# Performance work log

Measured on AMD Instinct MI355X. Metric: run time of the kernel, lower is better.

The kernel has to match this reference:

```python
import jax, jax.numpy as jnp
import numpy as np

N_NODES = 100000
N_EDGES = 1600000
NODE_FEAT_DIM = 140
NUM_OPCODES = 128
EMBED_DIM = 64
HIDDEN = 128
N_LAYERS = 4
LN_EPS = 1e-5


def _layer_norm(x, g, b):
    mu = jnp.mean(x, axis=-1, keepdims=True)
    var = jnp.mean(jnp.square(x - mu), axis=-1, keepdims=True)
    return (x - mu) * jax.lax.rsqrt(var + LN_EPS) * g + b


def setup_inputs() -> dict:
    key = jax.random.key(0)
    ks = jax.random.split(key, 16)
    node_feat = jax.random.normal(ks[0], (N_NODES, NODE_FEAT_DIM), dtype=jnp.float32)
    node_opcode = jax.random.randint(ks[1], (N_NODES,), 0, NUM_OPCODES)
    topo_depth = jax.random.uniform(ks[2], (N_NODES, 1), dtype=jnp.float32)
    edge_index = jax.random.randint(ks[3], (2, N_EDGES), 0, N_NODES)
    in_dim = NODE_FEAT_DIM + EMBED_DIM + 1  # 205
    s_in = 1.0 / np.sqrt(in_dim)
    s_h = 1.0 / np.sqrt(HIDDEN)
    embed = jax.random.normal(ks[4], (NUM_OPCODES, EMBED_DIM), dtype=jnp.float32)
    embed = embed.at[0].set(0.0)  # padding_idx=0
    W_in = jax.random.uniform(ks[5], (in_dim, HIDDEN), minval=-s_in, maxval=s_in, dtype=jnp.float32)
    b_in = jax.random.uniform(ks[6], (HIDDEN,), minval=-s_in, maxval=s_in, dtype=jnp.float32)
    ln0_g = jnp.ones((HIDDEN,), jnp.float32)
    ln0_b = jnp.zeros((HIDDEN,), jnp.float32)
    # SAGEConv per layer: lin_l (neighbors, with bias), lin_r (self, no bias)
    Wl = jax.random.uniform(ks[7], (N_LAYERS, HIDDEN, HIDDEN), minval=-s_h, maxval=s_h, dtype=jnp.float32)
    bl = jax.random.uniform(ks[8], (N_LAYERS, HIDDEN), minval=-s_h, maxval=s_h, dtype=jnp.float32)
    Wr = jax.random.uniform(ks[9], (N_LAYERS, HIDDEN, HIDDEN), minval=-s_h, maxval=s_h, dtype=jnp.float32)
    ln_g = jnp.ones((N_LAYERS, HIDDEN), jnp.float32)
    ln_b = jnp.zeros((N_LAYERS, HIDDEN), jnp.float32)
    return {"node_feat": node_feat, "topo_depth": topo_depth, "embed": embed,
            "W_in": W_in, "b_in": b_in, "ln0_g": ln0_g, "ln0_b": ln0_b,
            "Wl": Wl, "bl": bl, "Wr": Wr, "ln_g": ln_g, "ln_b": ln_b,
            "node_opcode": node_opcode, "edge_index": edge_index}


def reference(node_feat, topo_depth, embed, W_in, b_in, ln0_g, ln0_b,
              Wl, bl, Wr, ln_g, ln_b, node_opcode, edge_index):
    n = node_feat.shape[0]
    op = jnp.clip(node_opcode, 0, embed.shape[0] - 1)
    h = jnp.concatenate([node_feat, embed[op], topo_depth], axis=-1)  # (n, 205)
    # input_proj: Linear -> LayerNorm -> GELU (dropout = eval identity)
    h = jax.nn.gelu(_layer_norm(h @ W_in + b_in, ln0_g, ln0_b), approximate=False)
    src, tgt = edge_index[0], edge_index[1]
    deg = jax.ops.segment_sum(jnp.ones((src.shape[0],), h.dtype), tgt, num_segments=n)
    inv_deg = (1.0 / jnp.maximum(deg, 1.0))[:, None]
    for i in range(N_LAYERS):
        # mean-SAGE: aggregate source features onto targets
        agg = jax.ops.segment_sum(h[src], tgt, num_segments=n) * inv_deg
        out = agg @ Wl[i] + bl[i] + h @ Wr[i]
        h = _layer_norm(h + jax.nn.gelu(out, approximate=False), ln_g[i], ln_b[i])
    return h
```

## Files before the change

### kernel.cpp

```cpp
#include <hip/hip_runtime.h>
#include <cstdint>
#include <cstddef>

#define NN 100000
#define NE 1600000
#define FEAT 140
#define EMB 64
#define HID 128
#define LN_EPS 1e-5f
#define SCAN_NBLK 98
#define BK_SHIFT 9
#define NBUCK 196
#define MAXSEG 20480

typedef unsigned int uint;
typedef unsigned short ushort;
using short8 = __attribute__((ext_vector_type(8))) short;
using f32x4  = __attribute__((ext_vector_type(4))) float;

__device__ __forceinline__ float gelu_exact(float x) {
    return 0.5f * x * (1.0f + erff(x * 0.70710678118654752440f));
}

__device__ __forceinline__ ushort f2bf(float f) {
    uint u = __float_as_uint(f);
    uint r = (u + 0x7fff + ((u >> 16) & 1)) >> 16;
    return (ushort)r;
}

__device__ __forceinline__ float bf2f(ushort u) {
    return __uint_as_float(((uint)u) << 16);
}

__device__ __forceinline__ float bflo(uint u) {
    return __uint_as_float(u << 16);
}
__device__ __forceinline__ float bfhi(uint u) {
    return __uint_as_float(u & 0xffff0000u);
}

__global__ __launch_bounds__(256) void pack_weights_kernel(
    const float* __restrict__ W_in, const float* __restrict__ Wl,
    const float* __restrict__ Wr,
    ushort* __restrict__ winp, ushort* __restrict__ wcat)
{
    const int tid = blockIdx.x * 256 + threadIdx.x;
    const int NIN = 7 * 8 * 64;
    const int NL  = 8 * 8 * 64;
    if (tid < NIN) {
        const int kk = tid >> 9;
        const int c  = (tid >> 6) & 7;
        const int l  = tid & 63;
        const int kbase = kk * 32 + (l >> 4) * 8;
        const int col = c * 16 + (l & 15);
        short8 v;
        #pragma unroll
        for (int j = 0; j < 8; ++j) {
            const int k = kbase + j;
            v[j] = (k < 205) ? (short)f2bf(W_in[k * 128 + col]) : (short)0;
        }
        *(short8*)(winp + (size_t)tid * 8) = v;
    } else if (tid < NIN + 4 * NL) {
        const int t2 = tid - NIN;
        const int layer = t2 >> 12;
        const int r = t2 & (NL - 1);
        const int kk = r >> 9;
        const int c  = (r >> 6) & 7;
        const int l  = r & 63;
        const int kbase = kk * 32 + (l >> 4) * 8;
        const int col = c * 16 + (l & 15);
        short8 v;
        #pragma unroll
        for (int j = 0; j < 8; ++j) {
            const int k = kbase + j;
            const float x = (k < 128)
                ? Wl[(size_t)layer * 16384 + k * 128 + col]
                : Wr[(size_t)layer * 16384 + (k - 128) * 128 + col];
            v[j] = (short)f2bf(x);
        }
        *(short8*)(wcat + (size_t)t2 * 8) = v;
    }
}

__global__ __launch_bounds__(256) void input_proj_mfma(
    const float* __restrict__ nf, const float* __restrict__ topo,
    const float* __restrict__ embed, const int* __restrict__ opcode,
    const ushort* __restrict__ Wp, const float* __restrict__ b_in,
    const float* __restrict__ g0, const float* __restrict__ b0,
    float* __restrict__ h_out, ushort* __restrict__ hb_out)
{
    __shared__ ushort xs[64 * 232];
    const int t = threadIdx.x;
    const int node0 = blockIdx.x * 64;

    for (int idx = t; idx < 64 * 35; idx += 256) {
        const int row = idx / 35, c = idx - row * 35;
        const int node = min(node0 + row, NN - 1);
        const float4 v = ((const float4*)nf)[(size_t)node * 35 + c];
        ushort* p = &xs[row * 232 + c * 4];
        p[0] = f2bf(v.x); p[1] = f2bf(v.y); p[2] = f2bf(v.z); p[3] = f2bf(v.w);
    }
    for (int idx = t; idx < 64 * 16; idx += 256) {
        const int row = idx >> 4, c = idx & 15;
        const int node = min(node0 + row, NN - 1);
        int op = opcode[node];
        op = min(max(op, 0), 127);
        const float4 v = ((const float4*)embed)[op * 16 + c];
        ushort* p = &xs[row * 232 + 140 + c * 4];
        p[0] = f2bf(v.x); p[1] = f2bf(v.y); p[2] = f2bf(v.z); p[3] = f2bf(v.w);
    }
    if (t < 64) {
        const int node = min(node0 + t, NN - 1);
        xs[t * 232 + 204] = f2bf(topo[node]);
    }
    for (int idx = t; idx < 64 * 19; idx += 256) {
        const int row = idx / 19, c = 205 + (idx - row * 19);
        xs[row * 232 + c] = 0;
    }
    __syncthreads();

    const int w = t >> 6, l = t & 63;
    const int gq = l >> 4, li = l & 15;

    f32x4 acc[8];
    #pragma unroll
    for (int c = 0; c < 8; ++c) acc[c] = (f32x4){0.f, 0.f, 0.f, 0.f};

    const short8* Bp = (const short8*)Wp;
    for (int kk = 0; kk < 7; ++kk) {
        const short8 a = *(const short8*)&xs[(w * 16 + li) * 232 + kk * 32 + gq * 8];
        #pragma unroll
        for (int c = 0; c < 8; ++c) {
            const short8 b = Bp[(kk * 8 + c) * 64 + l];
            acc[c] = __builtin_amdgcn_mfma_f32_16x16x32_bf16(a, b, acc[c], 0, 0, 0);
        }
    }

    float bias[8], gam[8], bet[8];
    #pragma unroll
    for (int c = 0; c < 8; ++c) {
        bias[c] = b_in[c * 16 + li];
        gam[c]  = g0[c * 16 + li];
        bet[c]  = b0[c * 16 + li];
    }
    float s[4] = {0, 0, 0, 0}, q[4] = {0, 0, 0, 0};
    #pragma unroll
    for (int c = 0; c < 8; ++c)
        #pragma unroll
        for (int r = 0; r < 4; ++r) {
            const float u = acc[c][r] + bias[c];
            acc[c][r] = u;
            s[r] += u;
            q[r] += u * u;
        }
    #pragma unroll
    for (int off = 1; off < 16; off <<= 1)
        #pragma unroll
        for (int r = 0; r < 4; ++r) {
            s[r] += __shfl_xor(s[r], off);
            q[r] += __shfl_xor(q[r], off);
        }
    #pragma unroll
    for (int r = 0; r < 4; ++r) {
        const int node = node0 + w * 16 + gq * 4 + r;
        if (node >= NN) continue;
        const float mean = s[r] * (1.0f / HID);
        const float var  = q[r] * (1.0f / HID) - mean * mean;
        const float rstd = rsqrtf(var + LN_EPS);
        #pragma unroll
        for (int c = 0; c < 8; ++c) {
            const float y = gelu_exact((acc[c][r] - mean) * rstd * gam[c] + bet[c]);
            h_out[(size_t)node * 128 + c * 16 + li] = y;
            hb_out[(size_t)node * 128 + c * 16 + li] = f2bf(y);
        }
    }
}

__global__ __launch_bounds__(256) void degree_hist_kernel(const int* __restrict__ tgt,
                                                          int* __restrict__ deg,
                                                          int* __restrict__ bhist) {
    __shared__ int lh[NBUCK];
    for (int i = threadIdx.x; i < NBUCK; i += 256) lh[i] = 0;
    __syncthreads();
    const int e0 = blockIdx.x * 2048;
    const int eend = min(e0 + 2048, NE);
    for (int e = e0 + threadIdx.x; e < eend; e += 256) {
        const int tv = tgt[e];
        atomicAdd(&deg[tv], 1);
        atomicAdd(&lh[tv >> BK_SHIFT], 1);
    }
    __syncthreads();
    for (int i = threadIdx.x; i < NBUCK; i += 256)
        if (lh[i]) atomicAdd(&bhist[i], lh[i]);
}

__global__ __launch_bounds__(256) void bucket_scan_kernel(const int* __restrict__ bhist,
                                                          int* __restrict__ bpos,
                                                          int* __restrict__ bcur) {
    __shared__ int s_[256];
    const int t = threadIdx.x;
    int v = (t < NBUCK) ? bhist[t] : 0;
    s_[t] = v;
    __syncthreads();
    for (int off = 1; off < 256; off <<= 1) {
        int u = (t >= off) ? s_[t - off] : 0;
        __syncthreads();
        s_[t] += u;
        __syncthreads();
    }
    if (t < NBUCK) { bpos[t] = s_[t] - v; bcur[t] = s_[t] - v; }
}

__global__ __launch_bounds__(256) void partition_kernel(const int* __restrict__ src,
                                                        const int* __restrict__ tgt,
                                                        int* __restrict__ bcur,
                                                        uint2* __restrict__ pairs) {
    __shared__ int lh[NBUCK];
    __shared__ int gbase[NBUCK];
    for (int i = threadIdx.x; i < NBUCK; i += 256) lh[i] = 0;
    __syncthreads();
    const int e0 = blockIdx.x * 2048;
    const int eend = min(e0 + 2048, NE);
    int myb[8], myr[8], mys[8], myt[8];
    int cnt = 0;
    for (int e = e0 + threadIdx.x; e < eend; e += 256) {
        const int tv = tgt[e];
        const int b = tv >> BK_SHIFT;
        myb[cnt] = b; myt[cnt] = tv; mys[cnt] = src[e];
        myr[cnt] = atomicAdd(&lh[b], 1);
        ++cnt;
    }
    __syncthreads();
    for (int i = threadIdx.x; i < NBUCK; i += 256)
        gbase[i] = lh[i] ? atomicAdd(&bcur[i], lh[i]) : 0;
    __syncthreads();
    for (int i = 0; i < cnt; ++i)
        pairs[gbase[myb[i]] + myr[i]] = make_uint2((uint)myt[i], (uint)mys[i]);
}

__global__ __launch_bounds__(256) void bucket_fill_kernel(const uint2* __restrict__ pairs,
                                                          const int* __restrict__ bpos,
                                                          const int* __restrict__ bhist,
                                                          const int* __restrict__ offs,
                                                          int* __restrict__ csr) {
    __shared__ int loffs[513];
    __shared__ int lcur[512];
    __shared__ int stage[MAXSEG];
    const int b = blockIdx.x;
    const int n0 = b << BK_SHIFT;
    const int nend = min(n0 + 512, NN);
    const int nn = nend - n0;
    for (int i = threadIdx.x; i <= nn; i += 256) loffs[i] = offs[n0 + i];
    for (int i = threadIdx.x; i < nn; i += 256) lcur[i] = 0;
    __syncthreads();
    const int base0 = loffs[0];
    const int seglen = loffs[nn] - base0;
    const int p0 = bpos[b], pc = bhist[b];
    if (seglen <= MAXSEG) {
        for (int i = threadIdx.x; i < pc; i += 256) {
            const uint2 pr = pairs[p0 + i];
            const int ln = (int)pr.x - n0;
            const int p = atomicAdd(&lcur[ln], 1);
            stage[loffs[ln] - base0 + p] = (int)pr.y;
        }
        __syncthreads();
        for (int i = threadIdx.x; i < seglen; i += 256) csr[base0 + i] = stage[i];
    } else {
        for (int i = threadIdx.x; i < pc; i += 256) {
            const uint2 pr = pairs[p0 + i];
            const int ln = (int)pr.x - n0;
            const int p = atomicAdd(&lcur[ln], 1);
            csr[loffs[ln] + p] = (int)pr.y;
        }
    }
}

__global__ __launch_bounds__(1024) void deg_reduce_kernel(const int* __restrict__ deg,
                                                          int* __restrict__ bsum) {
    const int i = blockIdx.x * 1024 + threadIdx.x;
    int v = (i < NN) ? deg[i] : 0;
    #pragma unroll
    for (int off = 32; off >= 1; off >>= 1) v += __shfl_down(v, off);
    __shared__ int wsum[16];
    const int lane = threadIdx.x & 63, wid = threadIdx.x >> 6;
    if (lane == 0) wsum[wid] = v;
    __syncthreads();
    if (threadIdx.x < 16) {
        int s = wsum[threadIdx.x];
        #pragma unroll
        for (int off = 8; off >= 1; off >>= 1) s += __shfl_down(s, off, 16);
        if (threadIdx.x == 0) bsum[blockIdx.x] = s;
    }
}

__global__ __launch_bounds__(128) void bsum_scan_kernel(const int* __restrict__ bsum,
                                                        int* __restrict__ boff,
                                                        int* __restrict__ offs) {
    __shared__ int s_[128];
    const int t = threadIdx.x;
    int v = (t < SCAN_NBLK) ? bsum[t] : 0;
    s_[t] = v;
    __syncthreads();
    for (int off = 1; off < 128; off <<= 1) {
        int u = (t >= off) ? s_[t - off] : 0;
        __syncthreads();
        s_[t] += u;
        __syncthreads();
    }
    if (t < SCAN_NBLK) boff[t] = s_[t] - v;
    if (t == 0) offs[NN] = NE;
}

__global__ __launch_bounds__(1024) void scan_apply_kernel(const int* __restrict__ deg,
                                                          const int* __restrict__ boff,
                                                          int* __restrict__ offs,
                                                          float* __restrict__ inv_deg) {
    const int i = blockIdx.x * 1024 + threadIdx.x;
    const int lane = threadIdx.x & 63, wid = threadIdx.x >> 6;
    int v = (i < NN) ? deg[i] : 0;
    int x = v;
    #pragma unroll
    for (int off = 1; off < 64; off <<= 1) {
        int y = __shfl_up(x, off);
        if (lane >= off) x += y;
    }
    __shared__ int wsum[16];
    __shared__ int woff[16];
    if (lane == 63) wsum[wid] = x;
    __syncthreads();
    if (threadIdx.x < 16) {
        const int own = wsum[threadIdx.x];
        int s = own;
        #pragma unroll
        for (int off = 1; off < 16; off <<= 1) {
            int y = __shfl_up(s, off, 16);
            if (threadIdx.x >= off) s += y;
        }
        woff[threadIdx.x] = s - own;
    }
    __syncthreads();
    if (i < NN) {
        const int ex = (x - v) + woff[wid] + boff[blockIdx.x];
        offs[i] = ex;
        inv_deg[i] = 1.0f / fmaxf((float)v, 1.0f);
    }
}

__global__ __launch_bounds__(256) void gather_kernel(const ushort* __restrict__ hb,
                                                     const int* __restrict__ csr,
                                                     const int* __restrict__ offs,
                                                     const float* __restrict__ inv_deg,
                                                     ushort* __restrict__ aggb) {
    const int node = blockIdx.x * 4 + (threadIdx.x >> 6);
    const int lane = threadIdx.x & 63;
    if (node >= NN) return;
    const int beg = offs[node];
    const int end = offs[node + 1];
    const uint* hp = (const uint*)hb;
    float ax = 0.0f, ay = 0.0f;
    int j = beg;
    for (; j + 8 <= end; j += 8) {
        int s0 = csr[j + 0], s1 = csr[j + 1], s2 = csr[j + 2], s3 = csr[j + 3];
        int s4 = csr[j + 4], s5 = csr[j + 5], s6 = csr[j + 6], s7 = csr[j + 7];
        uint u0 = hp[(size_t)s0 * 64 + lane];
        uint u1 = hp[(size_t)s1 * 64 + lane];
        uint u2 = hp[(size_t)s2 * 64 + lane];
        uint u3 = hp[(size_t)s3 * 64 + lane];
        uint u4 = hp[(size_t)s4 * 64 + lane];
        uint u5 = hp[(size_t)s5 * 64 + lane];
        uint u6 = hp[(size_t)s6 * 64 + lane];
        uint u7 = hp[(size_t)s7 * 64 + lane];
        float ax0 = bflo(u0) + bflo(u1);
        float ax1 = bflo(u2) + bflo(u3);
        float ax2 = bflo(u4) + bflo(u5);
        float ax3 = bflo(u6) + bflo(u7);
        float ay0 = bfhi(u0) + bfhi(u1);
        float ay1 = bfhi(u2) + bfhi(u3);
        float ay2 = bfhi(u4) + bfhi(u5);
        float ay3 = bfhi(u6) + bfhi(u7);
        ax += (ax0 + ax1) + (ax2 + ax3);
        ay += (ay0 + ay1) + (ay2 + ay3);
    }
    for (; j + 2 <= end; j += 2) {
        int s0 = csr[j + 0], s1 = csr[j + 1];
        uint u0 = hp[(size_t)s0 * 64 + lane];
        uint u1 = hp[(size_t)s1 * 64 + lane];
        ax += bflo(u0) + bflo(u1);
        ay += bfhi(u0) + bfhi(u1);
    }
    if (j < end) {
        uint u0 = hp[(size_t)csr[j] * 64 + lane];
        ax += bflo(u0);
        ay += bfhi(u0);
    }
    const float id = inv_deg[node];
    const uint lo = f2bf(ax * id);
    const uint hi = f2bf(ay * id);
    ((uint*)aggb)[(size_t)node * 64 + lane] = lo | (hi << 16);
}

__global__ __launch_bounds__(256) void layer_mfma(
    float* __restrict__ h, ushort* __restrict__ hb,
    const ushort* __restrict__ aggb, const ushort* __restrict__ Wp,
    const float* __restrict__ bl,
    const float* __restrict__ g, const float* __restrict__ b)
{
    const int t = threadIdx.x;
    const int w = t >> 6, l = t & 63;
    const int gq = l >> 4, li = l & 15;
    const int node0 = blockIdx.x * 64;
    const int ar = min(node0 + w * 16 + li, NN - 1);

    f32x4 acc[8];
    #pragma unroll
    for (int c = 0; c < 8; ++c) acc[c] = (f32x4){0.f, 0.f, 0.f, 0.f};

    const short8* Bp = (const short8*)Wp;
    const short8* Ag = (const short8*)aggb;
    const short8* Hg = (const short8*)hb;
    #pragma unroll
    for (int kk = 0; kk < 8; ++kk) {
        const short8 a = (kk < 4) ? Ag[(size_t)ar * 16 + kk * 4 + gq]
                                  : Hg[(size_t)ar * 16 + (kk - 4) * 4 + gq];
        #pragma unroll
        for (int c = 0; c < 8; ++c) {
            const short8 bf = Bp[(kk * 8 + c) * 64 + l];
            acc[c] = __builtin_amdgcn_mfma_f32_16x16x32_bf16(a, bf, acc[c], 0, 0, 0);
        }
    }

    float bias[8], gam[8], bet[8];
    #pragma unroll
    for (int c = 0; c < 8; ++c) {
        bias[c] = bl[c * 16 + li];
        gam[c]  = g[c * 16 + li];
        bet[c]  = b[c * 16 + li];
    }
    float s[4] = {0, 0, 0, 0}, q[4] = {0, 0, 0, 0};
    #pragma unroll
    for (int r = 0; r < 4; ++r) {
        const int nd = min(node0 + w * 16 + gq * 4 + r, NN - 1);
        #pragma unroll
        for (int c = 0; c < 8; ++c) {
            const float hv = h[(size_t)nd * 128 + c * 16 + li];
            const float tv = hv + gelu_exact(acc[c][r] + bias[c]);
            acc[c][r] = tv;
            s[r] += tv;
            q[r] += tv * tv;
        }
    }
    #pragma unroll
    for (int off = 1; off < 16; off <<= 1)
        #pragma unroll
        for (int r = 0; r < 4; ++r) {
            s[r] += __shfl_xor(s[r], off);
            q[r] += __shfl_xor(q[r], off);
        }
    #pragma unroll
    for (int r = 0; r < 4; ++r) {
        const int node = node0 + w * 16 + gq * 4 + r;
        if (node >= NN) continue;
        const float mean = s[r] * (1.0f / HID);
        const float var  = q[r] * (1.0f / HID) - mean * mean;
        const float rstd = rsqrtf(var + LN_EPS);
        #pragma unroll
        for (int c = 0; c < 8; ++c) {
            const float y = (acc[c][r] - mean) * rstd * gam[c] + bet[c];
            h[(size_t)node * 128 + c * 16 + li] = y;
            hb[(size_t)node * 128 + c * 16 + li] = f2bf(y);
        }
    }
}

extern "C" void kernel_launch(void* const* d_in, const int* in_sizes, int n_in,
                              void* d_out, int out_size, void* d_ws, size_t ws_size,
                              hipStream_t stream) {
    const float* node_feat = (const float*)d_in[0];
    const float* topo      = (const float*)d_in[1];
    const float* embed     = (const float*)d_in[2];
    const float* W_in      = (const float*)d_in[3];
    const float* b_in      = (const float*)d_in[4];
    const float* ln0_g     = (const float*)d_in[5];
    const float* ln0_b     = (const float*)d_in[6];
    const float* Wl        = (const float*)d_in[7];
    const float* bl        = (const float*)d_in[8];
    const float* Wr        = (const float*)d_in[9];
    const float* ln_g      = (const float*)d_in[10];
    const float* ln_b      = (const float*)d_in[11];
    const int*   opcode    = (const int*)d_in[12];
    const int*   edge      = (const int*)d_in[13];
    const int*   e_src = edge;
    const int*   e_tgt = edge + NE;

    float* h = (float*)d_out;

    char* w = (char*)d_ws;
    ushort* hb     = (ushort*)w;  w += (size_t)NN * HID * sizeof(ushort);
    ushort* aggb   = (ushort*)w;  w += (size_t)NN * HID * sizeof(ushort);
    float* inv_deg = (float*)w;   w += 400016;
    int*   deg_i   = (int*)w;     w += 400016;
    int*   offs    = (int*)w;     w += 400016;
    int*   bsum    = (int*)w;     w += 1024;
    int*   boff    = (int*)w;     w += 1024;
    int*   bhist   = (int*)w;     w += 1024;
    int*   bpos    = (int*)w;     w += 1024;
    int*   bcur    = (int*)w;     w += 1024;
    int*   csr     = (int*)w;     w += (size_t)NE * sizeof(int);
    uint2* pairs   = (uint2*)w;   w += (size_t)NE * sizeof(uint2);
    ushort* winp   = (ushort*)w;  w += 7 * 8 * 64 * 8 * sizeof(ushort);
    ushort* wcat   = (ushort*)w;  w += 4 * 8 * 8 * 64 * 8 * sizeof(ushort);

    const int EBLK = (NE + 2047) / 2048;

    pack_weights_kernel<<<78, 256, 0, stream>>>(W_in, Wl, Wr, winp, wcat);

    input_proj_mfma<<<(NN + 63) / 64, 256, 0, stream>>>(
        node_feat, topo, embed, opcode, winp, b_in, ln0_g, ln0_b, h, hb);

    hipMemsetAsync(deg_i, 0, (size_t)NN * sizeof(int), stream);
    hipMemsetAsync(bhist, 0, NBUCK * sizeof(int), stream);
    degree_hist_kernel<<<EBLK, 256, 0, stream>>>(e_tgt, deg_i, bhist);
    bucket_scan_kernel<<<1, 256, 0, stream>>>(bhist, bpos, bcur);
    deg_reduce_kernel<<<SCAN_NBLK, 1024, 0, stream>>>(deg_i, bsum);
    bsum_scan_kernel<<<1, 128, 0, stream>>>(bsum, boff, offs);
    scan_apply_kernel<<<SCAN_NBLK, 1024, 0, stream>>>(deg_i, boff, offs, inv_deg);
    partition_kernel<<<EBLK, 256, 0, stream>>>(e_src, e_tgt, bcur, pairs);
    bucket_fill_kernel<<<NBUCK, 256, 0, stream>>>(pairs, bpos, bhist, offs, csr);

    for (int layer = 0; layer < 4; ++layer) {
        gather_kernel<<<NN / 4, 256, 0, stream>>>(hb, csr, offs, inv_deg, aggb);
        layer_mfma<<<(NN + 63) / 64, 256, 0, stream>>>(
            h, hb, aggb, wcat + (size_t)layer * 8 * 8 * 64 * 8,
            bl + (size_t)layer * HID,
            ln_g + (size_t)layer * HID, ln_b + (size_t)layer * HID);
    }
}
```

Measured before the change: 651.2 us.

## Compute degrees in bucket fill and drop fp32 hidden-state traffic

Per-node degrees, CSR offsets and inverse degrees are now computed inside the bucket fill kernel from per-bucket counts plus a local scan. This removes the global degree atomics, the memset and three scan kernels. The fp32 copy of the hidden state is no longer written or read between layers: the residual is read from the bf16 copy and fp32 output is written only in the last layer. This cuts global memory traffic and launches, but the residual now carries bf16 rounding error that accumulates across layers.

```diff
diff --git a/kernel.cpp b/kernel.cpp
--- a/kernel.cpp
+++ b/kernel.cpp
@@ -8,7 +8,6 @@
 #define EMB 64
 #define HID 128
 #define LN_EPS 1e-5f
-#define SCAN_NBLK 98
 #define BK_SHIFT 9
 #define NBUCK 196
 #define MAXSEG 20480
@@ -87,7 +86,7 @@
     const float* __restrict__ embed, const int* __restrict__ opcode,
     const ushort* __restrict__ Wp, const float* __restrict__ b_in,
     const float* __restrict__ g0, const float* __restrict__ b0,
-    float* __restrict__ h_out, ushort* __restrict__ hb_out)
+    ushort* __restrict__ hb_out)
 {
     __shared__ ushort xs[64 * 232];
     const int t = threadIdx.x;
@@ -170,25 +169,20 @@
         #pragma unroll
         for (int c = 0; c < 8; ++c) {
             const float y = gelu_exact((acc[c][r] - mean) * rstd * gam[c] + bet[c]);
-            h_out[(size_t)node * 128 + c * 16 + li] = y;
             hb_out[(size_t)node * 128 + c * 16 + li] = f2bf(y);
         }
     }
 }
 
-__global__ __launch_bounds__(256) void degree_hist_kernel(const int* __restrict__ tgt,
-                                                          int* __restrict__ deg,
-                                                          int* __restrict__ bhist) {
+__global__ __launch_bounds__(256) void hist_kernel(const int* __restrict__ tgt,
+                                                   int* __restrict__ bhist) {
     __shared__ int lh[NBUCK];
     for (int i = threadIdx.x; i < NBUCK; i += 256) lh[i] = 0;
     __syncthreads();
     const int e0 = blockIdx.x * 2048;
     const int eend = min(e0 + 2048, NE);
-    for (int e = e0 + threadIdx.x; e < eend; e += 256) {
-        const int tv = tgt[e];
-        atomicAdd(&deg[tv], 1);
-        atomicAdd(&lh[tv >> BK_SHIFT], 1);
-    }
+    for (int e = e0 + threadIdx.x; e < eend; e += 256)
+        atomicAdd(&lh[tgt[e] >> BK_SHIFT], 1);
     __syncthreads();
     for (int i = threadIdx.x; i < NBUCK; i += 256)
         if (lh[i]) atomicAdd(&bhist[i], lh[i]);
@@ -241,108 +235,61 @@
 __global__ __launch_bounds__(256) void bucket_fill_kernel(const uint2* __restrict__ pairs,
                                                           const int* __restrict__ bpos,
                                                           const int* __restrict__ bhist,
-                                                          const int* __restrict__ offs,
+                                                          int* __restrict__ offs,
+                                                          float* __restrict__ inv_deg,
                                                           int* __restrict__ csr) {
-    __shared__ int loffs[513];
-    __shared__ int lcur[512];
+    __shared__ int cnt[512];
+    __shared__ int pref[512];
+    __shared__ int ssum[256];
     __shared__ int stage[MAXSEG];
+    const int t = threadIdx.x;
     const int b = blockIdx.x;
     const int n0 = b << BK_SHIFT;
-    const int nend = min(n0 + 512, NN);
-    const int nn = nend - n0;
-    for (int i = threadIdx.x; i <= nn; i += 256) loffs[i] = offs[n0 + i];
-    for (int i = threadIdx.x; i < nn; i += 256) lcur[i] = 0;
-    __syncthreads();
-    const int base0 = loffs[0];
-    const int seglen = loffs[nn] - base0;
+    const int nn = min(512, NN - n0);
     const int p0 = bpos[b], pc = bhist[b];
-    if (seglen <= MAXSEG) {
-        for (int i = threadIdx.x; i < pc; i += 256) {
+
+    for (int i = t; i < 512; i += 256) cnt[i] = 0;
+    __syncthreads();
+    for (int i = t; i < pc; i += 256)
+        atomicAdd(&cnt[(int)pairs[p0 + i].x - n0], 1);
+    __syncthreads();
+    const int a0 = cnt[2 * t], a1 = cnt[2 * t + 1];
+    ssum[t] = a0 + a1;
+    __syncthreads();
+    for (int off = 1; off < 256; off <<= 1) {
+        int u = (t >= off) ? ssum[t - off] : 0;
+        __syncthreads();
+        ssum[t] += u;
+        __syncthreads();
+    }
+    const int ebase = ssum[t] - a0 - a1;
+    pref[2 * t] = ebase;
+    pref[2 * t + 1] = ebase + a0;
+    __syncthreads();
+    for (int i = t; i < nn; i += 256) {
+        offs[n0 + i] = p0 + pref[i];
+        inv_deg[n0 + i] = 1.0f / fmaxf((float)cnt[i], 1.0f);
+    }
+    if (b == NBUCK - 1 && t == 0) offs[NN] = NE;
+    __syncthreads();
+    for (int i = t; i < 512; i += 256) cnt[i] = 0;
+    __syncthreads();
+    if (pc <= MAXSEG) {
+        for (int i = t; i < pc; i += 256) {
             const uint2 pr = pairs[p0 + i];
             const int ln = (int)pr.x - n0;
-            const int p = atomicAdd(&lcur[ln], 1);
-            stage[loffs[ln] - base0 + p] = (int)pr.y;
+            const int p = atomicAdd(&cnt[ln], 1);
+            stage[pref[ln] + p] = (int)pr.y;
         }
         __syncthreads();
-        for (int i = threadIdx.x; i < seglen; i += 256) csr[base0 + i] = stage[i];
+        for (int i = t; i < pc; i += 256) csr[p0 + i] = stage[i];
     } else {
-        for (int i = threadIdx.x; i < pc; i += 256) {
+        for (int i = t; i < pc; i += 256) {
             const uint2 pr = pairs[p0 + i];
             const int ln = (int)pr.x - n0;
-            const int p = atomicAdd(&lcur[ln], 1);
-            csr[loffs[ln] + p] = (int)pr.y;
-        }
-    }
-}
-
-__global__ __launch_bounds__(1024) void deg_reduce_kernel(const int* __restrict__ deg,
-                                                          int* __restrict__ bsum) {
-    const int i = blockIdx.x * 1024 + threadIdx.x;
-    int v = (i < NN) ? deg[i] : 0;
-    #pragma unroll
-    for (int off = 32; off >= 1; off >>= 1) v += __shfl_down(v, off);
-    __shared__ int wsum[16];
-    const int lane = threadIdx.x & 63, wid = threadIdx.x >> 6;
-    if (lane == 0) wsum[wid] = v;
-    __syncthreads();
-    if (threadIdx.x < 16) {
-        int s = wsum[threadIdx.x];
-        #pragma unroll
-        for (int off = 8; off >= 1; off >>= 1) s += __shfl_down(s, off, 16);
-        if (threadIdx.x == 0) bsum[blockIdx.x] = s;
-    }
-}
-
-__global__ __launch_bounds__(128) void bsum_scan_kernel(const int* __restrict__ bsum,
-                                                        int* __restrict__ boff,
-                                                        int* __restrict__ offs) {
-    __shared__ int s_[128];
-    const int t = threadIdx.x;
-    int v = (t < SCAN_NBLK) ? bsum[t] : 0;
-    s_[t] = v;
-    __syncthreads();
-    for (int off = 1; off < 128; off <<= 1) {
-        int u = (t >= off) ? s_[t - off] : 0;
-        __syncthreads();
-        s_[t] += u;
-        __syncthreads();
-    }
-    if (t < SCAN_NBLK) boff[t] = s_[t] - v;
-    if (t == 0) offs[NN] = NE;
-}
-
-__global__ __launch_bounds__(1024) void scan_apply_kernel(const int* __restrict__ deg,
-                                                          const int* __restrict__ boff,
-                                                          int* __restrict__ offs,
-                                                          float* __restrict__ inv_deg) {
-    const int i = blockIdx.x * 1024 + threadIdx.x;
-    const int lane = threadIdx.x & 63, wid = threadIdx.x >> 6;
-    int v = (i < NN) ? deg[i] : 0;
-    int x = v;
-    #pragma unroll
-    for (int off = 1; off < 64; off <<= 1) {
-        int y = __shfl_up(x, off);
-        if (lane >= off) x += y;
-    }
-    __shared__ int wsum[16];
-    __shared__ int woff[16];
-    if (lane == 63) wsum[wid] = x;
-    __syncthreads();
-    if (threadIdx.x < 16) {
-        const int own = wsum[threadIdx.x];
-        int s = own;
-        #pragma unroll
-        for (int off = 1; off < 16; off <<= 1) {
-            int y = __shfl_up(s, off, 16);
-            if (threadIdx.x >= off) s += y;
-        }
-        woff[threadIdx.x] = s - own;
-    }
-    __syncthreads();
-    if (i < NN) {
-        const int ex = (x - v) + woff[wid] + boff[blockIdx.x];
-        offs[i] = ex;
-        inv_deg[i] = 1.0f / fmaxf((float)v, 1.0f);
+            const int p = atomicAdd(&cnt[ln], 1);
+            csr[p0 + pref[ln] + p] = (int)pr.y;
+        }
     }
 }
 
@@ -400,10 +347,10 @@
 }
 
 __global__ __launch_bounds__(256) void layer_mfma(
-    float* __restrict__ h, ushort* __restrict__ hb,
-    const ushort* __restrict__ aggb, const ushort* __restrict__ Wp,
-    const float* __restrict__ bl,
-    const float* __restrict__ g, const float* __restrict__ b)
+    ushort* __restrict__ hb, const ushort* __restrict__ aggb,
+    const ushort* __restrict__ Wp, const float* __restrict__ bl,
+    const float* __restrict__ g, const float* __restrict__ b,
+    float* __restrict__ hout, int write_f32)
 {
     const int t = threadIdx.x;
     const int w = t >> 6, l = t & 63;
@@ -442,7 +389,7 @@
         const int nd = min(node0 + w * 16 + gq * 4 + r, NN - 1);
         #pragma unroll
         for (int c = 0; c < 8; ++c) {
-            const float hv = h[(size_t)nd * 128 + c * 16 + li];
+            const float hv = bf2f(hb[(size_t)nd * 128 + c * 16 + li]);
             const float tv = hv + gelu_exact(acc[c][r] + bias[c]);
             acc[c][r] = tv;
             s[r] += tv;
@@ -466,8 +413,8 @@
         #pragma unroll
         for (int c = 0; c < 8; ++c) {
             const float y = (acc[c][r] - mean) * rstd * gam[c] + bet[c];
-            h[(size_t)node * 128 + c * 16 + li] = y;
             hb[(size_t)node * 128 + c * 16 + li] = f2bf(y);
+            if (write_f32) hout[(size_t)node * 128 + c * 16 + li] = y;
         }
     }
 }
@@ -498,10 +445,7 @@
     ushort* hb     = (ushort*)w;  w += (size_t)NN * HID * sizeof(ushort);
     ushort* aggb   = (ushort*)w;  w += (size_t)NN * HID * sizeof(ushort);
     float* inv_deg = (float*)w;   w += 400016;
-    int*   deg_i   = (int*)w;     w += 400016;
     int*   offs    = (int*)w;     w += 400016;
-    int*   bsum    = (int*)w;     w += 1024;
-    int*   boff    = (int*)w;     w += 1024;
     int*   bhist   = (int*)w;     w += 1024;
     int*   bpos    = (int*)w;     w += 1024;
     int*   bcur    = (int*)w;     w += 1024;
@@ -515,23 +459,20 @@
     pack_weights_kernel<<<78, 256, 0, stream>>>(W_in, Wl, Wr, winp, wcat);
 
     input_proj_mfma<<<(NN + 63) / 64, 256, 0, stream>>>(
-        node_feat, topo, embed, opcode, winp, b_in, ln0_g, ln0_b, h, hb);
-
-    hipMemsetAsync(deg_i, 0, (size_t)NN * sizeof(int), stream);
+        node_feat, topo, embed, opcode, winp, b_in, ln0_g, ln0_b, hb);
+
     hipMemsetAsync(bhist, 0, NBUCK * sizeof(int), stream);
-    degree_hist_kernel<<<EBLK, 256, 0, stream>>>(e_tgt, deg_i, bhist);
+    hist_kernel<<<EBLK, 256, 0, stream>>>(e_tgt, bhist);
     bucket_scan_kernel<<<1, 256, 0, stream>>>(bhist, bpos, bcur);
-    deg_reduce_kernel<<<SCAN_NBLK, 1024, 0, stream>>>(deg_i, bsum);
-    bsum_scan_kernel<<<1, 128, 0, stream>>>(bsum, boff, offs);
-    scan_apply_kernel<<<SCAN_NBLK, 1024, 0, stream>>>(deg_i, boff, offs, inv_deg);
     partition_kernel<<<EBLK, 256, 0, stream>>>(e_src, e_tgt, bcur, pairs);
-    bucket_fill_kernel<<<NBUCK, 256, 0, stream>>>(pairs, bpos, bhist, offs, csr);
+    bucket_fill_kernel<<<NBUCK, 256, 0, stream>>>(pairs, bpos, bhist, offs, inv_deg, csr);
 
     for (int layer = 0; layer < 4; ++layer) {
         gather_kernel<<<NN / 4, 256, 0, stream>>>(hb, csr, offs, inv_deg, aggb);
         layer_mfma<<<(NN + 63) / 64, 256, 0, stream>>>(
-            h, hb, aggb, wcat + (size_t)layer * 8 * 8 * 64 * 8,
+            hb, aggb, wcat + (size_t)layer * 8 * 8 * 64 * 8,
             bl + (size_t)layer * HID,
-            ln_g + (size_t)layer * HID, ln_b + (size_t)layer * HID);
-    }
-}
+            ln_g + (size_t)layer * HID, ln_b + (size_t)layer * HID,
+            h, layer == 3 ? 1 : 0);
+    }
+}
```

Result: faster. 576.4 us (-11.5%).
